# Performance work log

Measured on AMD Instinct MI355X. Metric: run time of the kernel, lower is better.

## Reference

```python
import jax, jax.numpy as jnp
import numpy as np

BATCH = 4096
FEAT = 1024
HID = 1024


def setup_inputs() -> dict:
    key = jax.random.key(0)
    ks = jax.random.split(key, 11)
    s_x = 1.0 / np.sqrt(FEAT)
    s_h = 1.0 / np.sqrt(HID)
    return {
        "x": jax.random.normal(ks[0], (BATCH, FEAT), jnp.float32),
        "h_prev": jax.random.normal(ks[1], (BATCH, HID), jnp.float32),
        "c_prev": jax.random.normal(ks[2], (BATCH, HID), jnp.float32),
        # Dense(3*hidden) on x and h (keras Dense: y = x @ W + b)
        "W_ifo_x": jax.random.normal(ks[3], (FEAT, 3 * HID), jnp.float32) * s_x,
        "b_ifo_x": jnp.zeros((3 * HID,), jnp.float32),
        "W_ifo_h": jax.random.normal(ks[4], (HID, 3 * HID), jnp.float32) * s_h,
        "b_ifo_h": jnp.zeros((3 * HID,), jnp.float32),
        # Dense(hidden) on x and h for candidate 'a'
        "W_b_x": jax.random.normal(ks[5], (FEAT, HID), jnp.float32) * s_x,
        "b_b_x": jnp.zeros((HID,), jnp.float32),
        "W_b_h": jax.random.normal(ks[6], (HID, HID), jnp.float32) * s_h,
        "b_b_h": jnp.zeros((HID,), jnp.float32),
    }


def reference(x, h_prev, c_prev, W_ifo_x, b_ifo_x, W_ifo_h, b_ifo_h,
              W_b_x, b_b_x, W_b_h, b_b_h):
    # Fused gate projections: [B, 3H]
    ifo = jax.nn.sigmoid(x @ W_ifo_x + b_ifo_x + h_prev @ W_ifo_h + b_ifo_h)
    i, f, o = jnp.split(ifo, 3, axis=-1)
    a = jnp.tanh(x @ W_b_x + b_b_x + h_prev @ W_b_h + b_b_h)
    c = i * a + f * c_prev
    h = o * jnp.tanh(c)
    return (h, c)
```

## Files before the change

### kernel.cpp

```cpp
#include <hip/hip_runtime.h>
#include <hip/hip_bf16.h>
#include <stdint.h>
#include <stddef.h>


#define BATCH 4096
#define FEAT  1024
#define HID   1024
#define NCAT  4096
#define KCAT  2048

typedef __attribute__((ext_vector_type(8))) __bf16 bf16x8;
typedef __attribute__((ext_vector_type(4))) float  floatx4;

__device__ __forceinline__ unsigned short f2bf(float f) {
    __hip_bfloat16 b = __float2bfloat16(f);
    return *reinterpret_cast<unsigned short*>(&b);
}
__device__ __forceinline__ void gl2lds16(const unsigned short* g, unsigned short* l) {
    __builtin_amdgcn_global_load_lds(
        (const __attribute__((address_space(1))) void*)g,
        (__attribute__((address_space(3))) void*)l, 16, 0, 0);
}

#define TP_PAD 72
__global__ __launch_bounds__(256)
void pack_all(const float* __restrict__ x, const float* __restrict__ h,
              const float* __restrict__ Wix, const float* __restrict__ Wih,
              const float* __restrict__ Wbx, const float* __restrict__ Wbh,
              unsigned short* __restrict__ Xcat, unsigned short* __restrict__ Wt) {
    __shared__ unsigned short tile[64 * TP_PAD];
    const int t = threadIdx.x;
    const int b = blockIdx.x;
    if (b < BATCH) {
        const int m = b;
        const float* src = (t < 128) ? (x + (size_t)m * FEAT + t * 8)
                                     : (h + (size_t)m * HID + (t - 128) * 8);
        float4 v0 = *(const float4*)src;
        float4 v1 = *(const float4*)(src + 4);
        union { unsigned short s16[8]; uint4 v; } pk;
        pk.s16[0] = f2bf(v0.x); pk.s16[1] = f2bf(v0.y);
        pk.s16[2] = f2bf(v0.z); pk.s16[3] = f2bf(v0.w);
        pk.s16[4] = f2bf(v1.x); pk.s16[5] = f2bf(v1.y);
        pk.s16[6] = f2bf(v1.z); pk.s16[7] = f2bf(v1.w);
        *(uint4*)(Xcat + (size_t)m * KCAT + t * 8) = pk.v;
        return;
    }
    const int tid = b - BATCH;
    const int k0  = (tid & 31) * 64;
    const int q0  = (tid >> 5) * 64;
    const float* src; int stride, cb;
    if (q0 < 3072) { src = (k0 < FEAT) ? Wix : Wih; stride = 3072; cb = q0; }
    else           { src = (k0 < FEAT) ? Wbx : Wbh; stride = 1024; cb = q0 - 3072; }
    const int krow = (k0 < FEAT) ? k0 : (k0 - FEAT);
    {
        int kl = t >> 2;
        int c0 = (t & 3) * 16;
        const float* s = src + (size_t)(krow + kl) * stride + cb + c0;
        union { unsigned short s16[16]; uint4 v[2]; } tmp;
#pragma unroll
        for (int u = 0; u < 16; u += 4) {
            float4 v = *(const float4*)(s + u);
            tmp.s16[u + 0] = f2bf(v.x); tmp.s16[u + 1] = f2bf(v.y);
            tmp.s16[u + 2] = f2bf(v.z); tmp.s16[u + 3] = f2bf(v.w);
        }
        *(uint4*)&tile[kl * TP_PAD + c0]     = tmp.v[0];
        *(uint4*)&tile[kl * TP_PAD + c0 + 8] = tmp.v[1];
    }
    __syncthreads();
    {
        int nl = t >> 2, seg = t & 3;
        int q = q0 + nl;
        int g, j;
        if (q < 3072) { g = q >> 10; j = q & 1023; }
        else          { g = 3;       j = q - 3072; }
        int np = ((j >> 4) << 6) + (g << 4) + (j & 15);
        union { unsigned short s16[16]; uint4 v[2]; } pk;
#pragma unroll
        for (int u = 0; u < 16; ++u)
            pk.s16[u] = tile[(seg * 16 + u) * TP_PAD + nl];
        uint4* dst = (uint4*)(Wt + (size_t)np * KCAT + k0 + seg * 16);
        dst[0] = pk.v[0];
        dst[1] = pk.v[1];
    }
}

#define BM 128
#define BN 128
#define BK 32

__global__ __launch_bounds__(256)
void lstm_fused(const unsigned short* __restrict__ Xcat,
                const unsigned short* __restrict__ Wt,
                const float* __restrict__ c_prev,
                const float* __restrict__ bix, const float* __restrict__ bih,
                const float* __restrict__ bbx, const float* __restrict__ bbh,
                float* __restrict__ out_h, float* __restrict__ out_c) {
    __shared__ unsigned short As[BM * BK];
    __shared__ unsigned short Bs[BN * BK];
    const int t    = threadIdx.x;
    const int lane = t & 63;
    const int wave = t >> 6;
    const int wm   = (wave >> 1) * 64;
    const int wn   = (wave & 1) * 64;
    const int m0   = blockIdx.y * BM;
    const int n0   = blockIdx.x * BN;

    floatx4 acc[4][4];
#pragma unroll
    for (int i = 0; i < 4; ++i)
#pragma unroll
        for (int g = 0; g < 4; ++g) acc[i][g] = (floatx4){0.f, 0.f, 0.f, 0.f};

    const int lrow = t >> 2;
    const int cg   = ((t & 3) ^ (lrow + (lrow >> 2))) & 3;
    const int lcol = cg * 8;

    const int lm  = lane & 15;
    const int fcs = ((lane >> 4) ^ (lm + (lm >> 2))) & 3;

    for (int kk = 0; kk < KCAT; kk += BK) {
        __syncthreads();
        gl2lds16(Xcat + (size_t)(m0 + lrow)      * KCAT + kk + lcol, &As[t * 8]);
        gl2lds16(Xcat + (size_t)(m0 + lrow + 64) * KCAT + kk + lcol, &As[t * 8 + 2048]);
        gl2lds16(Wt   + (size_t)(n0 + lrow)      * KCAT + kk + lcol, &Bs[t * 8]);
        gl2lds16(Wt   + (size_t)(n0 + lrow + 64) * KCAT + kk + lcol, &Bs[t * 8 + 2048]);
        __syncthreads();

        bf16x8 a[4], b[4];
#pragma unroll
        for (int i = 0; i < 4; ++i)
            a[i] = *(const bf16x8*)&As[(wm + i * 16 + lm) * BK + fcs * 8];
#pragma unroll
        for (int g = 0; g < 4; ++g)
            b[g] = *(const bf16x8*)&Bs[(wn + g * 16 + lm) * BK + fcs * 8];
#pragma unroll
        for (int i = 0; i < 4; ++i)
#pragma unroll
            for (int g = 0; g < 4; ++g)
                acc[i][g] = __builtin_amdgcn_mfma_f32_16x16x32_bf16(a[i], b[g], acc[i][g], 0, 0, 0);
    }

    const int j  = (((n0 + wn) >> 6) << 4) + lm;
    const float bi = bix[j]           + bih[j];
    const float bf = bix[HID + j]     + bih[HID + j];
    const float bo = bix[2 * HID + j] + bih[2 * HID + j];
    const float ba = bbx[j]           + bbh[j];
#pragma unroll
    for (int i = 0; i < 4; ++i) {
#pragma unroll
        for (int r = 0; r < 4; ++r) {
            int m = m0 + wm + i * 16 + ((lane >> 4) * 4) + r;
            float pi = acc[i][0][r] + bi;
            float pf = acc[i][1][r] + bf;
            float po = acc[i][2][r] + bo;
            float pa = acc[i][3][r] + ba;
            float ig = 1.f / (1.f + __expf(-pi));
            float fg = 1.f / (1.f + __expf(-pf));
            float og = 1.f / (1.f + __expf(-po));
            float av = 2.f / (1.f + __expf(-2.f * pa)) - 1.f;
            float cp = c_prev[(size_t)m * HID + j];
            float cv = ig * av + fg * cp;
            float hv = og * (2.f / (1.f + __expf(-2.f * cv)) - 1.f);
            out_h[(size_t)m * HID + j] = hv;
            out_c[(size_t)m * HID + j] = cv;
        }
    }
}

__global__ void naive_lstm(const float* __restrict__ x, const float* __restrict__ h,
                           const float* __restrict__ cvp,
                           const float* __restrict__ Wix, const float* __restrict__ bix,
                           const float* __restrict__ Wih, const float* __restrict__ bih,
                           const float* __restrict__ Wbx, const float* __restrict__ bbx,
                           const float* __restrict__ Wbh, const float* __restrict__ bbh,
                           float* __restrict__ out_h, float* __restrict__ out_c) {
    const int j = blockIdx.x * 256 + threadIdx.x;
    const int m = blockIdx.y;
    float ai = 0.f, af = 0.f, ao = 0.f, aa = 0.f;
    for (int k = 0; k < FEAT; ++k) {
        float xk = x[(size_t)m * FEAT + k];
        ai += xk * Wix[(size_t)k * 3072 + j];
        af += xk * Wix[(size_t)k * 3072 + HID + j];
        ao += xk * Wix[(size_t)k * 3072 + 2 * HID + j];
        aa += xk * Wbx[(size_t)k * HID + j];
    }
    for (int k = 0; k < HID; ++k) {
        float hk = h[(size_t)m * HID + k];
        ai += hk * Wih[(size_t)k * 3072 + j];
        af += hk * Wih[(size_t)k * 3072 + HID + j];
        ao += hk * Wih[(size_t)k * 3072 + 2 * HID + j];
        aa += hk * Wbh[(size_t)k * HID + j];
    }
    ai += bix[j] + bih[j];
    af += bix[HID + j] + bih[HID + j];
    ao += bix[2 * HID + j] + bih[2 * HID + j];
    aa += bbx[j] + bbh[j];
    float ig = 1.f / (1.f + __expf(-ai));
    float fg = 1.f / (1.f + __expf(-af));
    float og = 1.f / (1.f + __expf(-ao));
    float av = 2.f / (1.f + __expf(-2.f * aa)) - 1.f;
    float cp = cvp[(size_t)m * HID + j];
    float cc = ig * av + fg * cp;
    float hh = og * (2.f / (1.f + __expf(-2.f * cc)) - 1.f);
    out_h[(size_t)m * HID + j] = hh;
    out_c[(size_t)m * HID + j] = cc;
}

extern "C" void kernel_launch(void* const* d_in, const int* in_sizes, int n_in,
                              void* d_out, int out_size, void* d_ws, size_t ws_size,
                              hipStream_t stream) {
    const float* x   = (const float*)d_in[0];
    const float* h   = (const float*)d_in[1];
    const float* c   = (const float*)d_in[2];
    const float* Wix = (const float*)d_in[3];
    const float* bix = (const float*)d_in[4];
    const float* Wih = (const float*)d_in[5];
    const float* bih = (const float*)d_in[6];
    const float* Wbx = (const float*)d_in[7];
    const float* bbx = (const float*)d_in[8];
    const float* Wbh = (const float*)d_in[9];
    const float* bbh = (const float*)d_in[10];

    float* out_h = (float*)d_out;
    float* out_c = out_h + (size_t)BATCH * HID;

    const size_t WT_BYTES = (size_t)NCAT * KCAT * 2;
    const size_t XC_BYTES = (size_t)BATCH * KCAT * 2;
    if (ws_size >= WT_BYTES + XC_BYTES) {
        unsigned short* Wt   = (unsigned short*)d_ws;
        unsigned short* Xcat = (unsigned short*)((char*)d_ws + WT_BYTES);
        pack_all<<<BATCH + 2048, 256, 0, stream>>>(x, h, Wix, Wih, Wbx, Wbh, Xcat, Wt);
        lstm_fused<<<dim3(NCAT / BN, BATCH / BM), 256, 0, stream>>>(
            Xcat, Wt, c, bix, bih, bbx, bbh, out_h, out_c);
    } else {
        naive_lstm<<<dim3(HID / 256, BATCH), 256, 0, stream>>>(
            x, h, c, Wix, bix, Wih, bih, Wbx, bbx, Wbh, bbh, out_h, out_c);
    }
}
```

Measured before the change: 228.0 us.

## Enlarge GEMM tiles to 256x256x64 with double-buffered LDS prefetch

```diff
diff --git a/kernel.cpp b/kernel.cpp
--- a/kernel.cpp
+++ b/kernel.cpp
@@ -32,8 +32,8 @@
     __shared__ unsigned short tile[64 * TP_PAD];
     const int t = threadIdx.x;
     const int b = blockIdx.x;
-    if (b < BATCH) {
-        const int m = b;
+    if (b >= 2048) {
+        const int m = b - 2048;
         const float* src = (t < 128) ? (x + (size_t)m * FEAT + t * 8)
                                      : (h + (size_t)m * HID + (t - 128) * 8);
         float4 v0 = *(const float4*)src;
@@ -46,7 +46,7 @@
         *(uint4*)(Xcat + (size_t)m * KCAT + t * 8) = pk.v;
         return;
     }
-    const int tid = b - BATCH;
+    const int tid = b;
     const int k0  = (tid & 31) * 64;
     const int q0  = (tid >> 5) * 64;
     const float* src; int stride, cb;
@@ -85,60 +85,110 @@
     }
 }
 
-#define BM 128
-#define BN 128
-#define BK 32
-
-__global__ __launch_bounds__(256)
+#define BM 256
+#define BN 256
+#define BK 64
+#define KT (KCAT / BK)
+
+__device__ __forceinline__ void stage_kt(
+    const unsigned short* __restrict__ Xcat, const unsigned short* __restrict__ Wt,
+    unsigned short* __restrict__ Adst, unsigned short* __restrict__ Bdst,
+    int m0, int n0, int kko, int t) {
+#pragma unroll
+    for (int u = 0; u < 4; ++u) {
+        int slot = t + u * 512;
+        int row  = slot >> 3;
+        int sch  = ((slot & 7) ^ (row & 7)) * 8;
+        gl2lds16(Xcat + (size_t)(m0 + row) * KCAT + kko + sch, Adst + slot * 8);
+    }
+#pragma unroll
+    for (int u = 0; u < 4; ++u) {
+        int slot = t + u * 512;
+        int row  = slot >> 3;
+        int sch  = ((slot & 7) ^ (row & 7)) * 8;
+        gl2lds16(Wt + (size_t)(n0 + row) * KCAT + kko + sch, Bdst + slot * 8);
+    }
+}
+
+__global__ __launch_bounds__(512, 2)
 void lstm_fused(const unsigned short* __restrict__ Xcat,
                 const unsigned short* __restrict__ Wt,
                 const float* __restrict__ c_prev,
                 const float* __restrict__ bix, const float* __restrict__ bih,
                 const float* __restrict__ bbx, const float* __restrict__ bbh,
                 float* __restrict__ out_h, float* __restrict__ out_c) {
-    __shared__ unsigned short As[BM * BK];
-    __shared__ unsigned short Bs[BN * BK];
+    __shared__ unsigned short As[2][BM * BK];
+    __shared__ unsigned short Bs[2][BN * BK];
     const int t    = threadIdx.x;
     const int lane = t & 63;
-    const int wave = t >> 6;
-    const int wm   = (wave >> 1) * 64;
-    const int wn   = (wave & 1) * 64;
+    const int wid  = t >> 6;
+    const int wm   = (wid >> 2) * 128;
+    const int wn   = (wid & 3) * 64;
     const int m0   = blockIdx.y * BM;
     const int n0   = blockIdx.x * BN;
-
-    floatx4 acc[4][4];
-#pragma unroll
-    for (int i = 0; i < 4; ++i)
+    const int lm   = lane & 15;
+    const int lk   = lane >> 4;
+    const int lx   = lane & 7;
+
+    floatx4 acc[8][4];
+#pragma unroll
+    for (int i = 0; i < 8; ++i)
 #pragma unroll
         for (int g = 0; g < 4; ++g) acc[i][g] = (floatx4){0.f, 0.f, 0.f, 0.f};
 
-    const int lrow = t >> 2;
-    const int cg   = ((t & 3) ^ (lrow + (lrow >> 2))) & 3;
-    const int lcol = cg * 8;
-
-    const int lm  = lane & 15;
-    const int fcs = ((lane >> 4) ^ (lm + (lm >> 2))) & 3;
-
-    for (int kk = 0; kk < KCAT; kk += BK) {
-        __syncthreads();
-        gl2lds16(Xcat + (size_t)(m0 + lrow)      * KCAT + kk + lcol, &As[t * 8]);
-        gl2lds16(Xcat + (size_t)(m0 + lrow + 64) * KCAT + kk + lcol, &As[t * 8 + 2048]);
-        gl2lds16(Wt   + (size_t)(n0 + lrow)      * KCAT + kk + lcol, &Bs[t * 8]);
-        gl2lds16(Wt   + (size_t)(n0 + lrow + 64) * KCAT + kk + lcol, &Bs[t * 8 + 2048]);
-        __syncthreads();
-
-        bf16x8 a[4], b[4];
-#pragma unroll
-        for (int i = 0; i < 4; ++i)
-            a[i] = *(const bf16x8*)&As[(wm + i * 16 + lm) * BK + fcs * 8];
-#pragma unroll
-        for (int g = 0; g < 4; ++g)
-            b[g] = *(const bf16x8*)&Bs[(wn + g * 16 + lm) * BK + fcs * 8];
-#pragma unroll
-        for (int i = 0; i < 4; ++i)
-#pragma unroll
-            for (int g = 0; g < 4; ++g)
-                acc[i][g] = __builtin_amdgcn_mfma_f32_16x16x32_bf16(a[i], b[g], acc[i][g], 0, 0, 0);
+    stage_kt(Xcat, Wt, &As[0][0], &Bs[0][0], m0, n0, 0,  t);
+    stage_kt(Xcat, Wt, &As[1][0], &Bs[1][0], m0, n0, BK, t);
+    asm volatile("s_waitcnt vmcnt(8)" ::: "memory");
+    __builtin_amdgcn_s_barrier();
+    asm volatile("" ::: "memory");
+
+    for (int kt = 0; kt < KT; ++kt) {
+        const unsigned short* Ab = &As[kt & 1][0];
+        const unsigned short* Bb = &Bs[kt & 1][0];
+
+        bf16x8 bb[4][2];
+#pragma unroll
+        for (int g = 0; g < 4; ++g) {
+            int c = wn + g * 16 + lm;
+#pragma unroll
+            for (int ks = 0; ks < 2; ++ks)
+                bb[g][ks] = *(const bf16x8*)&Bb[c * BK + (((ks * 4 + lk) ^ lx) * 8)];
+        }
+#pragma unroll
+        for (int mh = 0; mh < 2; ++mh) {
+            bf16x8 aa[4][2];
+#pragma unroll
+            for (int i = 0; i < 4; ++i) {
+                int r = wm + mh * 64 + i * 16 + lm;
+#pragma unroll
+                for (int ks = 0; ks < 2; ++ks)
+                    aa[i][ks] = *(const bf16x8*)&Ab[r * BK + (((ks * 4 + lk) ^ lx) * 8)];
+            }
+            __builtin_amdgcn_s_setprio(1);
+#pragma unroll
+            for (int i = 0; i < 4; ++i)
+#pragma unroll
+                for (int g = 0; g < 4; ++g)
+#pragma unroll
+                    for (int ks = 0; ks < 2; ++ks)
+                        acc[mh * 4 + i][g] = __builtin_amdgcn_mfma_f32_16x16x32_bf16(
+                            aa[i][ks], bb[g][ks], acc[mh * 4 + i][g], 0, 0, 0);
+            __builtin_amdgcn_s_setprio(0);
+        }
+
+        if (kt + 1 < KT) {
+            asm volatile("" ::: "memory");
+            __builtin_amdgcn_s_barrier();
+            if (kt + 2 < KT) {
+                stage_kt(Xcat, Wt, &As[kt & 1][0], &Bs[kt & 1][0],
+                         m0, n0, (kt + 2) * BK, t);
+                asm volatile("s_waitcnt vmcnt(8)" ::: "memory");
+            } else {
+                asm volatile("s_waitcnt vmcnt(0)" ::: "memory");
+            }
+            __builtin_amdgcn_s_barrier();
+            asm volatile("" ::: "memory");
+        }
     }
 
     const int j  = (((n0 + wn) >> 6) << 4) + lm;
@@ -147,10 +197,10 @@
     const float bo = bix[2 * HID + j] + bih[2 * HID + j];
     const float ba = bbx[j]           + bbh[j];
 #pragma unroll
-    for (int i = 0; i < 4; ++i) {
+    for (int i = 0; i < 8; ++i) {
 #pragma unroll
         for (int r = 0; r < 4; ++r) {
-            int m = m0 + wm + i * 16 + ((lane >> 4) * 4) + r;
+            int m = m0 + wm + i * 16 + (lk * 4) + r;
             float pi = acc[i][0][r] + bi;
             float pf = acc[i][1][r] + bf;
             float po = acc[i][2][r] + bo;
@@ -231,7 +281,7 @@
         unsigned short* Wt   = (unsigned short*)d_ws;
         unsigned short* Xcat = (unsigned short*)((char*)d_ws + WT_BYTES);
         pack_all<<<BATCH + 2048, 256, 0, stream>>>(x, h, Wix, Wih, Wbx, Wbh, Xcat, Wt);
-        lstm_fused<<<dim3(NCAT / BN, BATCH / BM), 256, 0, stream>>>(
+        lstm_fused<<<dim3(NCAT / BN, BATCH / BM), 512, 0, stream>>>(
             Xcat, Wt, c, bix, bih, bbx, bbh, out_h, out_c);
     } else {
         naive_lstm<<<dim3(HID / 256, BATCH), 256, 0, stream>>>(
```

Result: faster. 206.1 us (-9.6%).

## Rewrite GEMM as 256x256 tiles with 8 waves and double-buffered LDS pipeline

Applied to the files above, without the earlier changes.

```diff
diff --git a/kernel.cpp b/kernel.cpp
--- a/kernel.cpp
+++ b/kernel.cpp
@@ -32,21 +32,25 @@
     __shared__ unsigned short tile[64 * TP_PAD];
     const int t = threadIdx.x;
     const int b = blockIdx.x;
-    if (b < BATCH) {
-        const int m = b;
-        const float* src = (t < 128) ? (x + (size_t)m * FEAT + t * 8)
-                                     : (h + (size_t)m * HID + (t - 128) * 8);
-        float4 v0 = *(const float4*)src;
-        float4 v1 = *(const float4*)(src + 4);
-        union { unsigned short s16[8]; uint4 v; } pk;
-        pk.s16[0] = f2bf(v0.x); pk.s16[1] = f2bf(v0.y);
-        pk.s16[2] = f2bf(v0.z); pk.s16[3] = f2bf(v0.w);
-        pk.s16[4] = f2bf(v1.x); pk.s16[5] = f2bf(v1.y);
-        pk.s16[6] = f2bf(v1.z); pk.s16[7] = f2bf(v1.w);
-        *(uint4*)(Xcat + (size_t)m * KCAT + t * 8) = pk.v;
+    if (b >= 2048) {
+        const int mbase = (b - 2048) * 4;
+#pragma unroll
+        for (int r = 0; r < 4; ++r) {
+            const int m = mbase + r;
+            const float* src = (t < 128) ? (x + (size_t)m * FEAT + t * 8)
+                                         : (h + (size_t)m * HID + (t - 128) * 8);
+            float4 v0 = *(const float4*)src;
+            float4 v1 = *(const float4*)(src + 4);
+            union { unsigned short s16[8]; uint4 v; } pk;
+            pk.s16[0] = f2bf(v0.x); pk.s16[1] = f2bf(v0.y);
+            pk.s16[2] = f2bf(v0.z); pk.s16[3] = f2bf(v0.w);
+            pk.s16[4] = f2bf(v1.x); pk.s16[5] = f2bf(v1.y);
+            pk.s16[6] = f2bf(v1.z); pk.s16[7] = f2bf(v1.w);
+            *(uint4*)(Xcat + (size_t)m * KCAT + t * 8) = pk.v;
+        }
         return;
     }
-    const int tid = b - BATCH;
+    const int tid = b;
     const int k0  = (tid & 31) * 64;
     const int q0  = (tid >> 5) * 64;
     const float* src; int stride, cb;
@@ -85,60 +89,121 @@
     }
 }
 
-#define BM 128
-#define BN 128
-#define BK 32
-
-__global__ __launch_bounds__(256)
+#define BM 256
+#define BN 256
+#define BK 64
+#define NIT 16
+#define HALF 8192
+
+#define A_OFF(PAR, KS) (((PAR) * 2 + (KS)) * HALF)
+#define B_OFF(PAR, KS) (32768 + ((PAR) * 2 + (KS)) * HALF)
+
+__device__ __forceinline__ void stage_half(
+    const unsigned short* __restrict__ src, int row0, int kt, int ks,
+    unsigned short* __restrict__ ldsbase, int t) {
+#pragma unroll
+    for (int u = 0; u < 2; ++u) {
+        int hslot = t + u * 512;
+        int row   = hslot >> 2;
+        int chofs = hslot & 3;
+        int c     = chofs ^ ((row >> 1) & 3);
+        gl2lds16(src + (size_t)(row0 + row) * KCAT + kt * BK + ks * 32 + c * 8,
+                 ldsbase + hslot * 8);
+    }
+}
+
+#define LOAD_BB(PAR, KS)                                                        \
+    _Pragma("unroll")                                                           \
+    for (int g = 0; g < 4; ++g)                                                 \
+        bb[g] = *(const bf16x8*)&lds[B_OFF(PAR, KS) + (wn + g * 16 + lm) * 32 + cr];
+#define LOAD_AA(PAR, KS, IQ)                                                    \
+    _Pragma("unroll")                                                           \
+    for (int ii = 0; ii < 4; ++ii)                                              \
+        aa[ii] = *(const bf16x8*)&lds[A_OFF(PAR, KS) + (wm + (IQ) * 64 + ii * 16 + lm) * 32 + cr];
+#define DO_MFMA(IQ)                                                             \
+    asm volatile("s_waitcnt lgkmcnt(0)" ::: "memory");                          \
+    __builtin_amdgcn_s_setprio(1);                                              \
+    _Pragma("unroll")                                                           \
+    for (int ii = 0; ii < 4; ++ii)                                              \
+        _Pragma("unroll")                                                       \
+        for (int g = 0; g < 4; ++g)                                             \
+            acc[(IQ) * 4 + ii][g] = __builtin_amdgcn_mfma_f32_16x16x32_bf16(    \
+                aa[ii], bb[g], acc[(IQ) * 4 + ii][g], 0, 0, 0);                 \
+    __builtin_amdgcn_s_setprio(0);
+#define BAR __builtin_amdgcn_s_barrier();
+
+__global__ __launch_bounds__(512, 2)
 void lstm_fused(const unsigned short* __restrict__ Xcat,
                 const unsigned short* __restrict__ Wt,
                 const float* __restrict__ c_prev,
                 const float* __restrict__ bix, const float* __restrict__ bih,
                 const float* __restrict__ bbx, const float* __restrict__ bbh,
                 float* __restrict__ out_h, float* __restrict__ out_c) {
-    __shared__ unsigned short As[BM * BK];
-    __shared__ unsigned short Bs[BN * BK];
+    __shared__ unsigned short lds[65536];
     const int t    = threadIdx.x;
     const int lane = t & 63;
-    const int wave = t >> 6;
-    const int wm   = (wave >> 1) * 64;
-    const int wn   = (wave & 1) * 64;
+    const int wid  = t >> 6;
+    const int wm   = (wid >> 2) * 128;
+    const int wn   = (wid & 3) * 64;
     const int m0   = blockIdx.y * BM;
     const int n0   = blockIdx.x * BN;
-
-    floatx4 acc[4][4];
-#pragma unroll
-    for (int i = 0; i < 4; ++i)
+    const int lm   = lane & 15;
+    const int lk   = lane >> 4;
+    const int cr   = (lk ^ ((lm >> 1) & 3)) * 8;
+
+    floatx4 acc[8][4];
+#pragma unroll
+    for (int i = 0; i < 8; ++i)
 #pragma unroll
         for (int g = 0; g < 4; ++g) acc[i][g] = (floatx4){0.f, 0.f, 0.f, 0.f};
 
-    const int lrow = t >> 2;
-    const int cg   = ((t & 3) ^ (lrow + (lrow >> 2))) & 3;
-    const int lcol = cg * 8;
-
-    const int lm  = lane & 15;
-    const int fcs = ((lane >> 4) ^ (lm + (lm >> 2))) & 3;
-
-    for (int kk = 0; kk < KCAT; kk += BK) {
-        __syncthreads();
-        gl2lds16(Xcat + (size_t)(m0 + lrow)      * KCAT + kk + lcol, &As[t * 8]);
-        gl2lds16(Xcat + (size_t)(m0 + lrow + 64) * KCAT + kk + lcol, &As[t * 8 + 2048]);
-        gl2lds16(Wt   + (size_t)(n0 + lrow)      * KCAT + kk + lcol, &Bs[t * 8]);
-        gl2lds16(Wt   + (size_t)(n0 + lrow + 64) * KCAT + kk + lcol, &Bs[t * 8 + 2048]);
-        __syncthreads();
-
-        bf16x8 a[4], b[4];
-#pragma unroll
-        for (int i = 0; i < 4; ++i)
-            a[i] = *(const bf16x8*)&As[(wm + i * 16 + lm) * BK + fcs * 8];
-#pragma unroll
-        for (int g = 0; g < 4; ++g)
-            b[g] = *(const bf16x8*)&Bs[(wn + g * 16 + lm) * BK + fcs * 8];
-#pragma unroll
-        for (int i = 0; i < 4; ++i)
-#pragma unroll
-            for (int g = 0; g < 4; ++g)
-                acc[i][g] = __builtin_amdgcn_mfma_f32_16x16x32_bf16(a[i], b[g], acc[i][g], 0, 0, 0);
+    stage_half(Xcat, m0, 0, 0, lds + A_OFF(0, 0), t);
+    stage_half(Wt,   n0, 0, 0, lds + B_OFF(0, 0), t);
+    stage_half(Xcat, m0, 0, 1, lds + A_OFF(0, 1), t);
+    stage_half(Wt,   n0, 0, 1, lds + B_OFF(0, 1), t);
+    stage_half(Xcat, m0, 1, 0, lds + A_OFF(1, 0), t);
+    stage_half(Wt,   n0, 1, 0, lds + B_OFF(1, 0), t);
+    asm volatile("s_waitcnt vmcnt(4)" ::: "memory");
+    BAR
+
+    bf16x8 aa[4], bb[4];
+
+    for (int it = 0; it < NIT; ++it) {
+        const int k1 = 2 * it + 1, k2 = 2 * it + 2, k3 = 2 * it + 3;
+        const bool more = (it < NIT - 1);
+
+        LOAD_BB(0, 0) LOAD_AA(0, 0, 0)
+        stage_half(Xcat, m0, k1, 1, lds + A_OFF(1, 1), t);
+        BAR DO_MFMA(0) BAR
+        LOAD_AA(0, 0, 1)
+        stage_half(Wt, n0, k1, 1, lds + B_OFF(1, 1), t);
+        BAR DO_MFMA(1) BAR
+        LOAD_BB(0, 1) LOAD_AA(0, 1, 0)
+        if (more) stage_half(Xcat, m0, k2, 0, lds + A_OFF(0, 0), t);
+        BAR DO_MFMA(0) BAR
+        LOAD_AA(0, 1, 1)
+        if (more) {
+            stage_half(Wt, n0, k2, 0, lds + B_OFF(0, 0), t);
+            asm volatile("s_waitcnt vmcnt(4)" ::: "memory");
+        } else {
+            asm volatile("s_waitcnt vmcnt(0)" ::: "memory");
+        }
+        BAR DO_MFMA(1) BAR
+        LOAD_BB(1, 0) LOAD_AA(1, 0, 0)
+        if (more) stage_half(Xcat, m0, k2, 1, lds + A_OFF(0, 1), t);
+        BAR DO_MFMA(0) BAR
+        LOAD_AA(1, 0, 1)
+        if (more) stage_half(Wt, n0, k2, 1, lds + B_OFF(0, 1), t);
+        BAR DO_MFMA(1) BAR
+        LOAD_BB(1, 1) LOAD_AA(1, 1, 0)
+        if (more) stage_half(Xcat, m0, k3, 0, lds + A_OFF(1, 0), t);
+        BAR DO_MFMA(0) BAR
+        LOAD_AA(1, 1, 1)
+        if (more) {
+            stage_half(Wt, n0, k3, 0, lds + B_OFF(1, 0), t);
+            asm volatile("s_waitcnt vmcnt(4)" ::: "memory");
+        }
+        BAR DO_MFMA(1) BAR
     }
 
     const int j  = (((n0 + wn) >> 6) << 4) + lm;
@@ -147,10 +212,10 @@
     const float bo = bix[2 * HID + j] + bih[2 * HID + j];
     const float ba = bbx[j]           + bbh[j];
 #pragma unroll
-    for (int i = 0; i < 4; ++i) {
+    for (int i = 0; i < 8; ++i) {
 #pragma unroll
         for (int r = 0; r < 4; ++r) {
-            int m = m0 + wm + i * 16 + ((lane >> 4) * 4) + r;
+            int m = m0 + wm + i * 16 + (lk * 4) + r;
             float pi = acc[i][0][r] + bi;
             float pf = acc[i][1][r] + bf;
             float po = acc[i][2][r] + bo;
@@ -230,8 +295,8 @@
     if (ws_size >= WT_BYTES + XC_BYTES) {
         unsigned short* Wt   = (unsigned short*)d_ws;
         unsigned short* Xcat = (unsigned short*)((char*)d_ws + WT_BYTES);
-        pack_all<<<BATCH + 2048, 256, 0, stream>>>(x, h, Wix, Wih, Wbx, Wbh, Xcat, Wt);
-        lstm_fused<<<dim3(NCAT / BN, BATCH / BM), 256, 0, stream>>>(
+        pack_all<<<2048 + 1024, 256, 0, stream>>>(x, h, Wix, Wih, Wbx, Wbh, Xcat, Wt);
+        lstm_fused<<<dim3(NCAT / BN, BATCH / BM), 512, 0, stream>>>(
             Xcat, Wt, c, bix, bih, bbx, bbh, out_h, out_c);
     } else {
         naive_lstm<<<dim3(HID / 256, BATCH), 256, 0, stream>>>(
```

New measurement: 200.2 us. 12.2% less time.

## Fuse activation bf16 conversion into GEMM with multi-stage LDS software pipeline

Applied to the files above, without the earlier changes.

```diff
diff --git a/kernel.cpp b/kernel.cpp
--- a/kernel.cpp
+++ b/kernel.cpp
@@ -25,28 +25,12 @@
 
 #define TP_PAD 72
 __global__ __launch_bounds__(256)
-void pack_all(const float* __restrict__ x, const float* __restrict__ h,
-              const float* __restrict__ Wix, const float* __restrict__ Wih,
-              const float* __restrict__ Wbx, const float* __restrict__ Wbh,
-              unsigned short* __restrict__ Xcat, unsigned short* __restrict__ Wt) {
+void pack_wt(const float* __restrict__ Wix, const float* __restrict__ Wih,
+             const float* __restrict__ Wbx, const float* __restrict__ Wbh,
+             unsigned short* __restrict__ Wt) {
     __shared__ unsigned short tile[64 * TP_PAD];
-    const int t = threadIdx.x;
-    const int b = blockIdx.x;
-    if (b < BATCH) {
-        const int m = b;
-        const float* src = (t < 128) ? (x + (size_t)m * FEAT + t * 8)
-                                     : (h + (size_t)m * HID + (t - 128) * 8);
-        float4 v0 = *(const float4*)src;
-        float4 v1 = *(const float4*)(src + 4);
-        union { unsigned short s16[8]; uint4 v; } pk;
-        pk.s16[0] = f2bf(v0.x); pk.s16[1] = f2bf(v0.y);
-        pk.s16[2] = f2bf(v0.z); pk.s16[3] = f2bf(v0.w);
-        pk.s16[4] = f2bf(v1.x); pk.s16[5] = f2bf(v1.y);
-        pk.s16[6] = f2bf(v1.z); pk.s16[7] = f2bf(v1.w);
-        *(uint4*)(Xcat + (size_t)m * KCAT + t * 8) = pk.v;
-        return;
-    }
-    const int tid = b - BATCH;
+    const int t   = threadIdx.x;
+    const int tid = blockIdx.x;
     const int k0  = (tid & 31) * 64;
     const int q0  = (tid >> 5) * 64;
     const float* src; int stride, cb;
@@ -55,8 +39,9 @@
     const int krow = (k0 < FEAT) ? k0 : (k0 - FEAT);
     {
         int kl = t >> 2;
-        int c0 = (t & 3) * 16;
-        const float* s = src + (size_t)(krow + kl) * stride + cb + c0;
+        int cc = t & 3;
+        int c0s = ((cc ^ (kl >> 4)) << 4);
+        const float* s = src + (size_t)(krow + kl) * stride + cb + cc * 16;
         union { unsigned short s16[16]; uint4 v[2]; } tmp;
 #pragma unroll
         for (int u = 0; u < 16; u += 4) {
@@ -64,8 +49,8 @@
             tmp.s16[u + 0] = f2bf(v.x); tmp.s16[u + 1] = f2bf(v.y);
             tmp.s16[u + 2] = f2bf(v.z); tmp.s16[u + 3] = f2bf(v.w);
         }
-        *(uint4*)&tile[kl * TP_PAD + c0]     = tmp.v[0];
-        *(uint4*)&tile[kl * TP_PAD + c0 + 8] = tmp.v[1];
+        *(uint4*)&tile[kl * TP_PAD + c0s]     = tmp.v[0];
+        *(uint4*)&tile[kl * TP_PAD + c0s + 8] = tmp.v[1];
     }
     __syncthreads();
     {
@@ -75,10 +60,11 @@
         if (q < 3072) { g = q >> 10; j = q & 1023; }
         else          { g = 3;       j = q - 3072; }
         int np = ((j >> 4) << 6) + (g << 4) + (j & 15);
+        int ccr = (((nl >> 4) ^ seg) << 4) + (nl & 15);
         union { unsigned short s16[16]; uint4 v[2]; } pk;
 #pragma unroll
         for (int u = 0; u < 16; ++u)
-            pk.s16[u] = tile[(seg * 16 + u) * TP_PAD + nl];
+            pk.s16[u] = tile[(seg * 16 + u) * TP_PAD + ccr];
         uint4* dst = (uint4*)(Wt + (size_t)np * KCAT + k0 + seg * 16);
         dst[0] = pk.v[0];
         dst[1] = pk.v[1];
@@ -87,24 +73,87 @@
 
 #define BM 128
 #define BN 128
-#define BK 32
-
-__global__ __launch_bounds__(256)
-void lstm_fused(const unsigned short* __restrict__ Xcat,
+#define BK 64
+#define NIT 16
+#define HALF 4096
+
+#define A_OFF(PAR, KS) (((PAR) * 2 + (KS)) * HALF)
+#define B_OFF(PAR, KS) (16384 + ((PAR) * 2 + (KS)) * HALF)
+
+#define ISSUE_A(S, KT, KS) {                                                    \
+    const float* s_ = ((KT) < 16) ? (xrow + (KT) * 64 + (KS) * 32)              \
+                                  : (hrow + ((KT) - 16) * 64 + (KS) * 32);      \
+    S[0] = *(const floatx4*)(s_);      S[1] = *(const floatx4*)(s_ + 4);        \
+    S[2] = *(const floatx4*)(s_ + 8);  S[3] = *(const floatx4*)(s_ + 12); }
+
+#define COMMIT_A(S, PAR, KS) {                                                  \
+    union { unsigned short u[8]; uint4 v; } w0_, w1_;                           \
+    _Pragma("unroll")                                                           \
+    for (int e_ = 0; e_ < 4; ++e_) {                                            \
+        w0_.u[e_] = f2bf(S[0][e_]); w0_.u[4 + e_] = f2bf(S[1][e_]);             \
+        w1_.u[e_] = f2bf(S[2][e_]); w1_.u[4 + e_] = f2bf(S[3][e_]); }           \
+    *(uint4*)&lds[A_OFF(PAR, KS) + am * 32 + as0 * 8] = w0_.v;                  \
+    *(uint4*)&lds[A_OFF(PAR, KS) + am * 32 + as1 * 8] = w1_.v; }
+
+__device__ __forceinline__ void stage_half(
+    const unsigned short* __restrict__ Wt, int n0, int kt, int ks,
+    unsigned short* __restrict__ ldsbase, int t) {
+#pragma unroll
+    for (int u = 0; u < 2; ++u) {
+        int hslot = t + u * 256;
+        int row   = hslot >> 2;
+        int c     = (hslot & 3) ^ ((row >> 1) & 3);
+        gl2lds16(Wt + (size_t)(n0 + row) * KCAT + kt * BK + ks * 32 + c * 8,
+                 ldsbase + hslot * 8);
+    }
+}
+
+#define LOAD_BB(PAR, KS)                                                        \
+    _Pragma("unroll")                                                           \
+    for (int g_ = 0; g_ < 4; ++g_)                                              \
+        bb[g_] = *(const bf16x8*)&lds[B_OFF(PAR, KS) + (wn + g_ * 16 + lm) * 32 + cr];
+#define LOAD_AA2(PAR, KS, IH)                                                   \
+    _Pragma("unroll")                                                           \
+    for (int ii = 0; ii < 2; ++ii)                                              \
+        aa[ii] = *(const bf16x8*)&lds[A_OFF(PAR, KS) + (wm + (IH) * 32 + ii * 16 + lm) * 32 + cr];
+#define MFMA8(IH)                                                               \
+    __builtin_amdgcn_s_setprio(1);                                              \
+    _Pragma("unroll")                                                           \
+    for (int ii = 0; ii < 2; ++ii)                                              \
+        _Pragma("unroll")                                                       \
+        for (int g_ = 0; g_ < 4; ++g_)                                          \
+            acc[(IH) * 2 + ii][g_] = __builtin_amdgcn_mfma_f32_16x16x32_bf16(   \
+                aa[ii], bb[g_], acc[(IH) * 2 + ii][g_], 0, 0, 0);               \
+    __builtin_amdgcn_s_setprio(0);
+#define BAR __builtin_amdgcn_s_barrier();
+#define WAITK(N) asm volatile("s_waitcnt lgkmcnt(" #N ")" ::: "memory");
+
+__global__ __launch_bounds__(256, 2)
+void lstm_fused(const float* __restrict__ x, const float* __restrict__ h,
                 const unsigned short* __restrict__ Wt,
                 const float* __restrict__ c_prev,
                 const float* __restrict__ bix, const float* __restrict__ bih,
                 const float* __restrict__ bbx, const float* __restrict__ bbh,
                 float* __restrict__ out_h, float* __restrict__ out_c) {
-    __shared__ unsigned short As[BM * BK];
-    __shared__ unsigned short Bs[BN * BK];
+    __shared__ unsigned short lds[32768];
     const int t    = threadIdx.x;
     const int lane = t & 63;
-    const int wave = t >> 6;
-    const int wm   = (wave >> 1) * 64;
-    const int wn   = (wave & 1) * 64;
+    const int wid  = t >> 6;
+    const int wm   = (wid >> 1) * 64;
+    const int wn   = (wid & 1) * 64;
     const int m0   = blockIdx.y * BM;
     const int n0   = blockIdx.x * BN;
+    const int lm   = lane & 15;
+    const int lk   = lane >> 4;
+    const int cr   = (lk ^ ((lm >> 1) & 3)) * 8;
+
+    const int am   = t >> 1;
+    const float* xrow = x + (size_t)(m0 + am) * FEAT + (t & 1) * 16;
+    const float* hrow = h + (size_t)(m0 + am) * HID  + (t & 1) * 16;
+    const int ac0  = (t & 1) * 2;
+    const int aswz = (am >> 1) & 3;
+    const int as0  = ac0 ^ aswz;
+    const int as1  = (ac0 + 1) ^ aswz;
 
     floatx4 acc[4][4];
 #pragma unroll
@@ -112,33 +161,53 @@
 #pragma unroll
         for (int g = 0; g < 4; ++g) acc[i][g] = (floatx4){0.f, 0.f, 0.f, 0.f};
 
-    const int lrow = t >> 2;
-    const int cg   = ((t & 3) ^ (lrow + (lrow >> 2))) & 3;
-    const int lcol = cg * 8;
-
-    const int lm  = lane & 15;
-    const int fcs = ((lane >> 4) ^ (lm + (lm >> 2))) & 3;
-
-    for (int kk = 0; kk < KCAT; kk += BK) {
-        __syncthreads();
-        gl2lds16(Xcat + (size_t)(m0 + lrow)      * KCAT + kk + lcol, &As[t * 8]);
-        gl2lds16(Xcat + (size_t)(m0 + lrow + 64) * KCAT + kk + lcol, &As[t * 8 + 2048]);
-        gl2lds16(Wt   + (size_t)(n0 + lrow)      * KCAT + kk + lcol, &Bs[t * 8]);
-        gl2lds16(Wt   + (size_t)(n0 + lrow + 64) * KCAT + kk + lcol, &Bs[t * 8 + 2048]);
-        __syncthreads();
-
-        bf16x8 a[4], b[4];
-#pragma unroll
-        for (int i = 0; i < 4; ++i)
-            a[i] = *(const bf16x8*)&As[(wm + i * 16 + lm) * BK + fcs * 8];
-#pragma unroll
-        for (int g = 0; g < 4; ++g)
-            b[g] = *(const bf16x8*)&Bs[(wn + g * 16 + lm) * BK + fcs * 8];
-#pragma unroll
-        for (int i = 0; i < 4; ++i)
-#pragma unroll
-            for (int g = 0; g < 4; ++g)
-                acc[i][g] = __builtin_amdgcn_mfma_f32_16x16x32_bf16(a[i], b[g], acc[i][g], 0, 0, 0);
+    floatx4 SO[4];
+    bf16x8 aa[2], bb[4];
+
+    ISSUE_A(SO, 0, 0) COMMIT_A(SO, 0, 0)
+    ISSUE_A(SO, 0, 1) COMMIT_A(SO, 0, 1)
+    ISSUE_A(SO, 1, 0) COMMIT_A(SO, 1, 0)
+    stage_half(Wt, n0, 0, 0, lds + B_OFF(0, 0), t);
+    stage_half(Wt, n0, 0, 1, lds + B_OFF(0, 1), t);
+    stage_half(Wt, n0, 1, 0, lds + B_OFF(1, 0), t);
+    stage_half(Wt, n0, 1, 1, lds + B_OFF(1, 1), t);
+    ISSUE_A(SO, 1, 1)
+    asm volatile("s_waitcnt vmcnt(4)" ::: "memory");
+    WAITK(0)
+    BAR
+
+    for (int it = 0; it < NIT; ++it) {
+        const int k2 = 2 * it + 2, k3 = 2 * it + 3;
+        const bool more = (it < NIT - 1);
+
+        COMMIT_A(SO, 1, 1)
+        LOAD_BB(0, 0) LOAD_AA2(0, 0, 0)
+        if (more) ISSUE_A(SO, k2, 0)
+        WAITK(6) BAR MFMA8(0) BAR
+        if (more) stage_half(Wt, n0, k2, 0, lds + B_OFF(0, 0), t);
+        LOAD_AA2(0, 0, 1)
+        BAR MFMA8(1) BAR
+        if (more) { COMMIT_A(SO, 0, 0) }
+        LOAD_BB(0, 1) LOAD_AA2(0, 1, 0)
+        if (more) ISSUE_A(SO, k2, 1)
+        WAITK(6) BAR MFMA8(0) BAR
+        if (more) stage_half(Wt, n0, k2, 1, lds + B_OFF(0, 1), t);
+        LOAD_AA2(0, 1, 1)
+        BAR MFMA8(1) BAR
+        if (more) { COMMIT_A(SO, 0, 1) }
+        LOAD_BB(1, 0) LOAD_AA2(1, 0, 0)
+        if (more) ISSUE_A(SO, k3, 0)
+        WAITK(6) BAR MFMA8(0) BAR
+        if (more) stage_half(Wt, n0, k3, 0, lds + B_OFF(1, 0), t);
+        LOAD_AA2(1, 0, 1)
+        BAR MFMA8(1) BAR
+        if (more) { COMMIT_A(SO, 1, 0) }
+        LOAD_BB(1, 1) LOAD_AA2(1, 1, 0)
+        if (more) ISSUE_A(SO, k3, 1)
+        WAITK(6) BAR MFMA8(0) BAR
+        if (more) stage_half(Wt, n0, k3, 1, lds + B_OFF(1, 1), t);
+        LOAD_AA2(1, 1, 1)
+        BAR MFMA8(1) BAR
     }
 
     const int j  = (((n0 + wn) >> 6) << 4) + lm;
@@ -150,7 +219,7 @@
     for (int i = 0; i < 4; ++i) {
 #pragma unroll
         for (int r = 0; r < 4; ++r) {
-            int m = m0 + wm + i * 16 + ((lane >> 4) * 4) + r;
+            int m = m0 + wm + i * 16 + (lk * 4) + r;
             float pi = acc[i][0][r] + bi;
             float pf = acc[i][1][r] + bf;
             float po = acc[i][2][r] + bo;
@@ -226,13 +295,11 @@
     float* out_c = out_h + (size_t)BATCH * HID;
 
     const size_t WT_BYTES = (size_t)NCAT * KCAT * 2;
-    const size_t XC_BYTES = (size_t)BATCH * KCAT * 2;
-    if (ws_size >= WT_BYTES + XC_BYTES) {
-        unsigned short* Wt   = (unsigned short*)d_ws;
-        unsigned short* Xcat = (unsigned short*)((char*)d_ws + WT_BYTES);
-        pack_all<<<BATCH + 2048, 256, 0, stream>>>(x, h, Wix, Wih, Wbx, Wbh, Xcat, Wt);
+    if (ws_size >= WT_BYTES) {
+        unsigned short* Wt = (unsigned short*)d_ws;
+        pack_wt<<<2048, 256, 0, stream>>>(Wix, Wih, Wbx, Wbh, Wt);
         lstm_fused<<<dim3(NCAT / BN, BATCH / BM), 256, 0, stream>>>(
-            Xcat, Wt, c, bix, bih, bbx, bbh, out_h, out_c);
+            x, h, Wt, c, bix, bih, bbx, bbh, out_h, out_c);
     } else {
         naive_lstm<<<dim3(HID / 256, BATCH), 256, 0, stream>>>(
             x, h, c, Wix, bix, Wih, bih, Wbx, bbx, Wbh, bbh, out_h, out_c);
```

Result: slower. 277.3 us (+21.6%).
